# Optimization experiments

Hardware: AMD Instinct MI355X
Metric: run time of the kernel (lower is better)

The kernel has to match this reference:

```python
import jax, jax.numpy as jnp
import numpy as np

B, S, D, H = 16, 1024, 768, 12
HD = D // H
SCALE = HD ** -0.5


def setup_inputs() -> dict:
    key = jax.random.key(0)
    k1, k2, k3, k4 = jax.random.split(key, 4)
    # Xavier-uniform-like init for the linear weights
    lim_qkv = (6.0 / (D + 3 * D)) ** 0.5
    lim_proj = (6.0 / (D + D)) ** 0.5
    return {
        "hidden_states": jax.random.normal(k1, (B, S, D), dtype=jnp.float32),
        "mask": jax.random.randint(k2, (B, S), 0, 2).astype(bool),
        "qkv_w": jax.random.uniform(k3, (3 * D, D), minval=-lim_qkv, maxval=lim_qkv, dtype=jnp.float32),
        "qkv_b": jnp.zeros((3 * D,), dtype=jnp.float32),
        "proj_w": jax.random.uniform(k4, (D, D), minval=-lim_proj, maxval=lim_proj, dtype=jnp.float32),
        "proj_b": jnp.zeros((D,), dtype=jnp.float32),
    }


def _masked_softmax(scores, attn_mask):
    # scores: [B,H,S,S]; attn_mask: [B,1,S,S] bool. Fully-masked rows -> all-zero
    # weights (torch gives NaN there but then zeroes the output rows; zeroing
    # the weights yields the identical final output without NaNs).
    neg_inf = jnp.finfo(scores.dtype).min
    m = jnp.max(jnp.where(attn_mask, scores, neg_inf), axis=-1, keepdims=True)
    e = jnp.where(attn_mask, jnp.exp(scores - m), 0.0)
    denom = jnp.sum(e, axis=-1, keepdims=True)
    return e / jnp.where(denom == 0, 1.0, denom)


def reference(hidden_states, mask, qkv_w, qkv_b, proj_w, proj_b):
    # fused QKV projection: [B,S,3D]
    qkv = hidden_states @ qkv_w.T + qkv_b
    qkv = qkv.reshape(B, S, 3, H, HD).transpose(2, 0, 3, 1, 4)  # [3,B,H,S,hd]
    q, k, v = qkv[0], qkv[1], qkv[2]
    tok_mask = mask[:, None, :, None]  # [B,1,S,1]
    q = jnp.where(tok_mask, q, 0.0)
    k = jnp.where(tok_mask, k, 0.0)
    v = jnp.where(tok_mask, v, 0.0)
    scores = jnp.einsum("bhqd,bhkd->bhqk", q, k) * SCALE
    attn_mask = (mask[:, :, None] & mask[:, None, :])[:, None]  # [B,1,S,S]
    attn = _masked_softmax(scores, attn_mask)
    context = jnp.einsum("bhqk,bhkd->bhqd", attn, v)
    context = context.transpose(0, 2, 1, 3).reshape(B, S, D)
    out = context @ proj_w.T + proj_b
    out = jnp.where(mask[:, :, None], out, 0.0)
    return out
```

## Files before the change

### kernel.cpp

```cpp
#include <hip/hip_runtime.h>
#include <cstdint>
#include <cstddef>

#define B 16
#define S 1024
#define D 768
#define H 12
#define HD 64
#define NTOK (B * S)
#define QKV_N (3 * D)
#define SCALE 0.125f
#define C2 2.88539008f
#define GK 768
#define NT_K 12

typedef _Float16 f16x8 __attribute__((ext_vector_type(8)));
typedef _Float16 f16x4 __attribute__((ext_vector_type(4)));
typedef __fp16 fp16x2 __attribute__((ext_vector_type(2)));
typedef float f32x4 __attribute__((ext_vector_type(4)));

typedef __attribute__((address_space(3))) void as3_void;
typedef const __attribute__((address_space(1))) void as1_void;

#if defined(__has_builtin)
#if __has_builtin(__builtin_amdgcn_exp2f)
#define EXP2(x) __builtin_amdgcn_exp2f(x)
#else
#define EXP2(x) exp2f(x)
#endif
#else
#define EXP2(x) exp2f(x)
#endif

#define BARRIER() asm volatile("s_barrier" ::: "memory")

__global__ __launch_bounds__(256) void normalize_mask_kernel(
    const unsigned char* __restrict__ raw, int* __restrict__ outm, int n) {
    __shared__ int s_isbyte;
    const int tid = threadIdx.x;
    if (tid == 0) s_isbyte = 0;
    __syncthreads();
    int found = 0;
    for (int i = tid; i < n; i += 256) {
        if ((i & 3) != 0 && raw[i] != 0) found = 1;
    }
    if (found) atomicOr(&s_isbyte, 1);
    __syncthreads();
    const int isbyte = s_isbyte;
    if (isbyte) {
        for (int i = tid; i < n; i += 256) outm[i] = raw[i] ? 1 : 0;
    } else {
        const int* r32 = (const int*)raw;
        for (int i = tid; i < n; i += 256) outm[i] = r32[i] ? 1 : 0;
    }
}

__global__ __launch_bounds__(256) void cvt_all_f16(
    const float* __restrict__ in0, _Float16* __restrict__ out0, int n0,
    const float* __restrict__ in1, _Float16* __restrict__ out1, int n1,
    const float* __restrict__ in2, _Float16* __restrict__ out2, int n2) {
    int i = blockIdx.x * 256 + threadIdx.x;
    const float* in;
    _Float16* out;
    if (i < n0) { in = in0; out = out0; }
    else if (i < n0 + n1) { i -= n0; in = in1; out = out1; }
    else { i -= n0 + n1; in = in2; out = out2; if (i >= n2) return; }
    const float4 v = ((const float4*)in)[i];
    f16x4 o;
    o[0] = (_Float16)v.x; o[1] = (_Float16)v.y;
    o[2] = (_Float16)v.z; o[3] = (_Float16)v.w;
    ((f16x4*)out)[i] = o;
}

template <int MODE>
__global__ __launch_bounds__(256, 2) void gemm16(
    const _Float16* __restrict__ A, const _Float16* __restrict__ Wm,
    const float* __restrict__ bias, const int* __restrict__ rowmask,
    int N, float* __restrict__ outf, _Float16* __restrict__ outh,
    _Float16* __restrict__ vtb) {
    __shared__ _Float16 smem[32768];

    const int tid = threadIdx.x;
    const int w = tid >> 6, l = tid & 63;
    const int wm = (w >> 1) * 64, wn = (w & 1) * 64;
    const int lg = l >> 4, lc = l & 15;

    const int bid = blockIdx.x;
    const int xcd = bid & 7;
    const int idx = bid >> 3;
    const int bn = (idx >> 4) * 128;
    const int bm = (xcd * 16 + (idx & 15)) * 128;

    f32x4 acc[4][4] = {};

#define STAGE(T, BUF)                                                           \
    {                                                                           \
        const int kt_ = (T) * 64;                                               \
        _Pragma("unroll")                                                       \
        for (int i_ = 0; i_ < 4; ++i_) {                                        \
            const int ci_ = (w << 2) + i_;                           \
            const int r_ = (ci_ << 3) + (l >> 3);                               \
            const int c16_ = (l & 7) ^ (r_ & 7);                                \
            __builtin_amdgcn_global_load_lds(                                   \
                (as1_void*)(A + (size_t)(bm + r_) * GK + kt_ + c16_ * 8),       \
                (as3_void*)(smem + (BUF) * 8192 + ci_ * 512), 16, 0, 0);        \
            __builtin_amdgcn_global_load_lds(                                   \
                (as1_void*)(Wm + (size_t)(bn + r_) * GK + kt_ + c16_ * 8),      \
                (as3_void*)(smem + 16384 + (BUF) * 8192 + ci_ * 512), 16, 0, 0);\
        }                                                                       \
    }

    STAGE(0, 0)

    for (int t = 0; t < NT_K; ++t) {
        const int cur = t & 1;
        if (t + 1 < NT_K) {
            STAGE(t + 1, cur ^ 1)
            asm volatile("s_waitcnt vmcnt(8)" ::: "memory");
        } else {
            asm volatile("s_waitcnt vmcnt(0)" ::: "memory");
        }
        BARRIER();

        const _Float16* sA = smem + cur * 8192;
        const _Float16* sB = smem + 16384 + cur * 8192;
        __builtin_amdgcn_s_setprio(1);
#pragma unroll
        for (int kk = 0; kk < 2; ++kk) {
            const int c16 = ((kk << 2) + lg) ^ (lc & 7);
            f16x8 af[4], bf[4];
#pragma unroll
            for (int ni = 0; ni < 4; ++ni)
                bf[ni] = *(const f16x8*)&sB[(wn + ni * 16 + lc) * 64 + c16 * 8];
#pragma unroll
            for (int mi = 0; mi < 4; ++mi)
                af[mi] = *(const f16x8*)&sA[(wm + mi * 16 + lc) * 64 + c16 * 8];
#pragma unroll
            for (int mi = 0; mi < 4; ++mi)
#pragma unroll
                for (int ni = 0; ni < 4; ++ni)
                    acc[mi][ni] = __builtin_amdgcn_mfma_f32_16x16x32_f16(
                        af[mi], bf[ni], acc[mi][ni], 0, 0, 0);
        }
        __builtin_amdgcn_s_setprio(0);
        BARRIER();
    }
#undef STAGE

    float bs[4];
#pragma unroll
    for (int ni = 0; ni < 4; ++ni) bs[ni] = bias[bn + wn + ni * 16 + lc];

    if (MODE == 1) {
        if (bn < 1536) {
#pragma unroll
            for (int mi = 0; mi < 4; ++mi) {
#pragma unroll
                for (int j = 0; j < 4; ++j) {
                    const int m = bm + wm + mi * 16 + lg * 4 + j;
#pragma unroll
                    for (int ni = 0; ni < 4; ++ni) {
                        const int col = bn + wn + ni * 16 + lc;
                        outh[(size_t)m * N + col] =
                            (_Float16)(acc[mi][ni][j] + bs[ni]);
                    }
                }
            }
        } else {
#pragma unroll
            for (int mi = 0; mi < 4; ++mi) {
#pragma unroll
                for (int ni = 0; ni < 4; ++ni) {
                    f16x4 v4;
#pragma unroll
                    for (int j = 0; j < 4; ++j)
                        v4[j] = (_Float16)(acc[mi][ni][j] + bs[ni]);
                    const int nl = wn + ni * 16 + lc;
                    const int ml = wm + mi * 16 + lg * 4;
                    *(f16x4*)&smem[nl * 136 + ml] = v4;
                }
            }
            __syncthreads();
            const int r = tid >> 1;
            const int c0 = (tid & 1) * 64;
            const int col0 = bn - 1536 + r;
            const int hh = col0 >> 6, hd = col0 & 63;
            const int bb = bm >> 10;
            const int s0 = (bm & 1023) + c0;
            _Float16* dst = vtb + ((size_t)(bb * H + hh) * HD + hd) * S + s0;
#pragma unroll
            for (int e = 0; e < 8; ++e)
                *(f16x8*)(dst + e * 8) = *(const f16x8*)&smem[r * 136 + c0 + e * 8];
        }
    } else {
#pragma unroll
        for (int mi = 0; mi < 4; ++mi) {
#pragma unroll
            for (int j = 0; j < 4; ++j) {
                const int m = bm + wm + mi * 16 + lg * 4 + j;
                const int mv = rowmask[m];
#pragma unroll
                for (int ni = 0; ni < 4; ++ni) {
                    const int col = bn + wn + ni * 16 + lc;
                    outf[(size_t)m * N + col] = mv ? acc[mi][ni][j] + bs[ni] : 0.f;
                }
            }
        }
    }
}

__global__ __launch_bounds__(256, 3) void attn_kernel(
    const _Float16* __restrict__ qkv, const _Float16* __restrict__ vtb,
    const int* __restrict__ mask, _Float16* __restrict__ ctx) {
    __shared__ _Float16 ksm[3][64 * 64];
    __shared__ _Float16 vsm[3][64 * 64];
    __shared__ float mbias[S];

    const int blk = blockIdx.x;
    const int xcd = blk & 7;
    const int idx = blk >> 3;
    const int bh_ = xcd * 24 + (idx >> 2);
    const int qt = idx & 3;
    const int h = bh_ % H;
    const int b = bh_ / H;
    const int tid = threadIdx.x;
    const int w = tid >> 6, lane = tid & 63;
    const int lg = lane >> 4, lc = lane & 15;

    const size_t bh = (size_t)(b * H + h);
    const _Float16* Kp = qkv + (size_t)(b * S) * QKV_N + D + h * HD;
    const _Float16* Vt = vtb + bh * HD * S;
    const int* mrow = mask + b * S;

    const int r0 = w * 8 + (lane >> 3);
    const int swz8 = ((lane & 7) ^ (r0 & 7)) * 8;
    const int koff0 = r0 * QKV_N + swz8;
    const int koff1 = (32 + r0) * QKV_N + swz8;
    const int voff0 = r0 * S + swz8;
    const int voff1 = (32 + r0) * S + swz8;

#define STAGE(T, BUF)                                                          \
    {                                                                          \
        const int kt_ = (T) * 64;                                              \
        __builtin_amdgcn_global_load_lds(                                      \
            (as1_void*)(Kp + (size_t)kt_ * QKV_N + koff0),                     \
            (as3_void*)(&ksm[BUF][w * 512]), 16, 0, 0);                        \
        __builtin_amdgcn_global_load_lds(                                      \
            (as1_void*)(Kp + (size_t)kt_ * QKV_N + koff1),                     \
            (as3_void*)(&ksm[BUF][2048 + w * 512]), 16, 0, 0);                 \
        __builtin_amdgcn_global_load_lds(                                      \
            (as1_void*)(Vt + (size_t)kt_ + voff0),                            \
            (as3_void*)(&vsm[BUF][w * 512]), 16, 0, 0);                        \
        __builtin_amdgcn_global_load_lds(                                      \
            (as1_void*)(Vt + (size_t)kt_ + voff1),                            \
            (as3_void*)(&vsm[BUF][2048 + w * 512]), 16, 0, 0);                 \
    }

    const int qbase = qt * 256 + w * 16 + lc;
    const _Float16 qs = (_Float16)(0.125f * 1.44269504f);
    f16x8 qf[4][2];
#pragma unroll
    for (int qg = 0; qg < 4; ++qg) {
        const _Float16* Qp =
            qkv + (size_t)(b * S + qbase + qg * 64) * QKV_N + h * HD;
        qf[qg][0] = *(const f16x8*)(Qp + lg * 8);
        qf[qg][1] = *(const f16x8*)(Qp + 32 + lg * 8);
        qf[qg][0] *= qs;
        qf[qg][1] *= qs;
    }

#pragma unroll
    for (int i = 0; i < 4; ++i)
        mbias[i * 256 + tid] = mrow[i * 256 + tid] ? -C2 : -1e9f;

    STAGE(0, 0)
    STAGE(1, 1)

    f32x4 acc[4][4] = {};
    float lsum[4] = {0.f, 0.f, 0.f, 0.f};
    fp16x2 ones;
    ones[0] = (__fp16)1.0f; ones[1] = (__fp16)1.0f;

    int cur = 0;
    for (int it = 0; it < S / 64; ++it) {
        if (it + 2 < S / 64) {
            int nb = cur + 2; if (nb >= 3) nb -= 3;
            STAGE(it + 2, nb)
        }
        if (it == 0)
            asm volatile("s_waitcnt vmcnt(8) lgkmcnt(0)" ::: "memory");
        else if (it + 2 < S / 64)
            asm volatile("s_waitcnt vmcnt(8)" ::: "memory");
        else if (it + 2 == S / 64)
            asm volatile("s_waitcnt vmcnt(4)" ::: "memory");
        else
            asm volatile("s_waitcnt vmcnt(0)" ::: "memory");
        BARRIER();

        __builtin_amdgcn_s_setprio(1);
#pragma unroll
        for (int u = 0; u < 2; ++u) {
            f16x8 pp8[4];
#pragma unroll
            for (int s = 0; s < 2; ++s) {
                const int t = 2 * u + s;
                const int krow = (t * 16 + lc) * 64;
                const f16x8 kfa =
                    *(const f16x8*)&ksm[cur][krow + (lg ^ (lc & 7)) * 8];
                const f16x8 kfb =
                    *(const f16x8*)&ksm[cur][krow + ((4 + lg) ^ (lc & 7)) * 8];
                const f32x4 mb = *(const f32x4*)&mbias[it * 64 + t * 16 + 4 * lg];
#pragma unroll
                for (int qg = 0; qg < 4; ++qg) {
                    f32x4 c = mb;
                    c = __builtin_amdgcn_mfma_f32_16x16x32_f16(kfa, qf[qg][0], c, 0, 0, 0);
                    c = __builtin_amdgcn_mfma_f32_16x16x32_f16(kfb, qf[qg][1], c, 0, 0, 0);
                    const auto u0 = __builtin_amdgcn_cvt_pkrtz(EXP2(c[0]), EXP2(c[1]));
                    const auto u1 = __builtin_amdgcn_cvt_pkrtz(EXP2(c[2]), EXP2(c[3]));
                    lsum[qg] = __builtin_amdgcn_fdot2(u0, ones, lsum[qg], false);
                    lsum[qg] = __builtin_amdgcn_fdot2(u1, ones, lsum[qg], false);
                    pp8[qg][s * 4 + 0] = (_Float16)u0[0];
                    pp8[qg][s * 4 + 1] = (_Float16)u0[1];
                    pp8[qg][s * 4 + 2] = (_Float16)u1[0];
                    pp8[qg][s * 4 + 3] = (_Float16)u1[1];
                }
            }

#pragma unroll
            for (int g = 0; g < 4; ++g) {
                const int vrow = (g * 16 + lc) * 64;
                const int cA = ((4 * u + (lg >> 1)) ^ (lc & 7)) * 8 + (lg & 1) * 4;
                const int cB = ((4 * u + 2 + (lg >> 1)) ^ (lc & 7)) * 8 + (lg & 1) * 4;
                const f16x4 vlo = *(const f16x4*)&vsm[cur][vrow + cA];
                const f16x4 vhi = *(const f16x4*)&vsm[cur][vrow + cB];
                f16x8 vf8;
                vf8[0] = vlo[0]; vf8[1] = vlo[1]; vf8[2] = vlo[2]; vf8[3] = vlo[3];
                vf8[4] = vhi[0]; vf8[5] = vhi[1]; vf8[6] = vhi[2]; vf8[7] = vhi[3];
#pragma unroll
                for (int qg = 0; qg < 4; ++qg)
                    acc[qg][g] = __builtin_amdgcn_mfma_f32_16x16x32_f16(
                        pp8[qg], vf8, acc[qg][g], 0, 0, 0);
            }
        }
        __builtin_amdgcn_s_setprio(0);
        BARRIER();
        if (++cur >= 3) cur = 0;
    }
#undef STAGE

#pragma unroll
    for (int qg = 0; qg < 4; ++qg) {
        float l = lsum[qg];
        l += __shfl_xor(l, 16);
        l += __shfl_xor(l, 32);
        const float inv = l > 0.f ? 1.f / l : 0.f;
#pragma unroll
        for (int j = 0; j < 4; ++j) {
            const int qin = 4 * lg + j;
            const float ij = __shfl(inv, qin);
            const int qr = qt * 256 + qg * 64 + w * 16 + qin;
            const float iq = mrow[qr] ? ij : 0.f;
            const size_t o = ((size_t)(b * S + qr)) * D + h * HD;
#pragma unroll
            for (int g = 0; g < 4; ++g)
                ctx[o + 16 * g + lc] = (_Float16)(acc[qg][g][j] * iq);
        }
    }
}

extern "C" void kernel_launch(void* const* d_in, const int* in_sizes, int n_in,
                              void* d_out, int out_size, void* d_ws, size_t ws_size,
                              hipStream_t stream) {
    const float* hidden = (const float*)d_in[0];
    const unsigned char* maskraw = (const unsigned char*)d_in[1];
    const float* qkv_w = (const float*)d_in[2];
    const float* qkv_b = (const float*)d_in[3];
    const float* proj_w = (const float*)d_in[4];
    const float* proj_b = (const float*)d_in[5];
    float* out = (float*)d_out;

    char* ws = (char*)d_ws;
    size_t off = 0;
    int* maskN = (int*)(ws + off);            off += (size_t)NTOK * 4;
    _Float16* hid16 = (_Float16*)(ws + off);  off += (size_t)NTOK * D * 2;
    _Float16* qkvw16 = (_Float16*)(ws + off); off += (size_t)QKV_N * D * 2;
    _Float16* projw16 = (_Float16*)(ws + off); off += (size_t)D * D * 2;
    _Float16* qkv16 = (_Float16*)(ws + off);  off += (size_t)NTOK * QKV_N * 2;
    _Float16* vt = (_Float16*)(ws + off);     off += (size_t)NTOK * D * 2;
    _Float16* ctx16 = (_Float16*)(ws + off);  off += (size_t)NTOK * D * 2;

    normalize_mask_kernel<<<1, 256, 0, stream>>>(maskraw, maskN, NTOK);

    const int n0 = NTOK * D / 4, n1 = QKV_N * D / 4, n2 = D * D / 4;
    cvt_all_f16<<<(n0 + n1 + n2 + 255) / 256, 256, 0, stream>>>(
        hidden, hid16, n0, qkv_w, qkvw16, n1, proj_w, projw16, n2);

    gemm16<1><<<dim3(2304), 256, 0, stream>>>(
        hid16, qkvw16, qkv_b, nullptr, QKV_N, nullptr, qkv16, vt);

    attn_kernel<<<dim3(B * H * (S / 256)), 256, 0, stream>>>(qkv16, vt, maskN, ctx16);

    gemm16<0><<<dim3(768), 256, 0, stream>>>(
        ctx16, projw16, proj_b, maskN, D, out, nullptr, nullptr);
}
```

Measured before the change: 191.1 us.

## Use 256x256 tiles with 512 threads for QKV GEMM and pack softmax probabilities

The QKV projection GEMM moves from 128x128 tiles with 256 threads to 256x256 tiles with 8 waves, each computing 128x64. This raises arithmetic intensity and cuts the number of global loads per FLOP. The V-transpose epilogue now runs in two passes through shared memory. Separately, the attention kernel packs the cvt_pkrtz results as 32-bit ints instead of inserting individual halves, which should avoid per-element register shuffles. The larger tile uses 128KB of LDS and more accumulator registers per block, and gives only 576 blocks, which risks lower occupancy and weaker tail balance.

```diff
diff --git a/kernel.cpp b/kernel.cpp
--- a/kernel.cpp
+++ b/kernel.cpp
@@ -18,6 +18,7 @@
 typedef _Float16 f16x4 __attribute__((ext_vector_type(4)));
 typedef __fp16 fp16x2 __attribute__((ext_vector_type(2)));
 typedef float f32x4 __attribute__((ext_vector_type(4)));
+typedef int i32x4 __attribute__((ext_vector_type(4)));
 
 typedef __attribute__((address_space(3))) void as3_void;
 typedef const __attribute__((address_space(1))) void as1_void;
@@ -33,6 +34,9 @@
 #endif
 
 #define BARRIER() asm volatile("s_barrier" ::: "memory")
+
+union PPack { f16x8 h; i32x4 i; };
+union CPack { fp16x2 h; int i; };
 
 __global__ __launch_bounds__(256) void normalize_mask_kernel(
     const unsigned char* __restrict__ raw, int* __restrict__ outm, int n) {
@@ -72,12 +76,140 @@
     ((f16x4*)out)[i] = o;
 }
 
-template <int MODE>
-__global__ __launch_bounds__(256, 2) void gemm16(
+__global__ __launch_bounds__(512, 2) void gemm256(
+    const _Float16* __restrict__ A, const _Float16* __restrict__ Wm,
+    const float* __restrict__ bias, _Float16* __restrict__ outh,
+    _Float16* __restrict__ vtb) {
+    __shared__ _Float16 smem[65536];
+
+    const int tid = threadIdx.x;
+    const int w = tid >> 6, l = tid & 63;
+    const int wr = w >> 2, wc = w & 3;
+    const int wm = wr * 128, wn = wc * 64;
+    const int lg = l >> 4, lc = l & 15;
+
+    const int bid = blockIdx.x;
+    const int xcd = bid & 7;
+    const int idx = bid >> 3;
+    const int bn = (idx >> 3) * 256;
+    const int bm = (xcd * 8 + (idx & 7)) * 256;
+
+    const int r0 = l >> 3;
+    const int sw8 = ((l & 7) ^ (l >> 3)) * 8;
+
+    f32x4 acc[8][4] = {};
+
+#define STG(T, BUF)                                                            \
+    {                                                                          \
+        const int kt_ = (T) * 64;                                              \
+        _Float16* sA_ = smem + (BUF) * 16384;                                  \
+        _Float16* sB_ = smem + 32768 + (BUF) * 16384;                          \
+        _Pragma("unroll")                                                      \
+        for (int i_ = 0; i_ < 4; ++i_) {                                       \
+            const int seg_ = i_ * 8 + w;                                       \
+            const int rr_ = seg_ * 8 + r0;                                     \
+            __builtin_amdgcn_global_load_lds(                                  \
+                (as1_void*)(A + (size_t)(bm + rr_) * GK + kt_ + sw8),          \
+                (as3_void*)(sA_ + seg_ * 512), 16, 0, 0);                      \
+            __builtin_amdgcn_global_load_lds(                                  \
+                (as1_void*)(Wm + (size_t)(bn + rr_) * GK + kt_ + sw8),         \
+                (as3_void*)(sB_ + seg_ * 512), 16, 0, 0);                      \
+        }                                                                      \
+    }
+
+    STG(0, 0)
+
+    for (int t = 0; t < NT_K; ++t) {
+        const int cur = t & 1;
+        if (t + 1 < NT_K) {
+            STG(t + 1, cur ^ 1)
+            asm volatile("s_waitcnt vmcnt(8)" ::: "memory");
+        } else {
+            asm volatile("s_waitcnt vmcnt(0)" ::: "memory");
+        }
+        BARRIER();
+
+        const _Float16* sA = smem + cur * 16384;
+        const _Float16* sB = smem + 32768 + cur * 16384;
+        __builtin_amdgcn_s_setprio(1);
+#pragma unroll
+        for (int kk = 0; kk < 2; ++kk) {
+            const int c16 = ((kk << 2) + lg) ^ (lc & 7);
+            f16x8 bf[4], af[8];
+#pragma unroll
+            for (int ni = 0; ni < 4; ++ni)
+                bf[ni] = *(const f16x8*)&sB[(wn + ni * 16 + lc) * 64 + c16 * 8];
+#pragma unroll
+            for (int mi = 0; mi < 8; ++mi)
+                af[mi] = *(const f16x8*)&sA[(wm + mi * 16 + lc) * 64 + c16 * 8];
+#pragma unroll
+            for (int mi = 0; mi < 8; ++mi)
+#pragma unroll
+                for (int ni = 0; ni < 4; ++ni)
+                    acc[mi][ni] = __builtin_amdgcn_mfma_f32_16x16x32_f16(
+                        af[mi], bf[ni], acc[mi][ni], 0, 0, 0);
+        }
+        __builtin_amdgcn_s_setprio(0);
+        BARRIER();
+    }
+#undef STG
+
+    float bs[4];
+#pragma unroll
+    for (int ni = 0; ni < 4; ++ni) bs[ni] = bias[bn + wn + ni * 16 + lc];
+
+    if (bn < 1536) {
+#pragma unroll
+        for (int mi = 0; mi < 8; ++mi) {
+#pragma unroll
+            for (int j = 0; j < 4; ++j) {
+                const int m = bm + wm + mi * 16 + lg * 4 + j;
+#pragma unroll
+                for (int ni = 0; ni < 4; ++ni) {
+                    const int col = bn + wn + ni * 16 + lc;
+                    outh[(size_t)m * QKV_N + col] =
+                        (_Float16)(acc[mi][ni][j] + bs[ni]);
+                }
+            }
+        }
+    } else {
+#pragma unroll
+        for (int p = 0; p < 2; ++p) {
+            BARRIER();
+            if ((wc >> 1) == p) {
+#pragma unroll
+                for (int mi = 0; mi < 8; ++mi) {
+#pragma unroll
+                    for (int ni = 0; ni < 4; ++ni) {
+                        f16x4 v4;
+#pragma unroll
+                        for (int j = 0; j < 4; ++j)
+                            v4[j] = (_Float16)(acc[mi][ni][j] + bs[ni]);
+                        const int cl = wn - p * 128 + ni * 16 + lc;
+                        const int row = wm + mi * 16 + lg * 4;
+                        *(f16x4*)&smem[cl * 264 + row] = v4;
+                    }
+                }
+            }
+            BARRIER();
+            const int r = tid >> 2;
+            const int c0 = (tid & 3) * 64;
+            const int col0 = bn - 1536 + p * 128 + r;
+            const int hh = col0 >> 6, hd = col0 & 63;
+            const int bb = bm >> 10;
+            const int s0 = (bm & 1023) + c0;
+            _Float16* dst = vtb + ((size_t)(bb * H + hh) * HD + hd) * S + s0;
+#pragma unroll
+            for (int e = 0; e < 8; ++e)
+                *(f16x8*)(dst + e * 8) = *(const f16x8*)&smem[r * 264 + c0 + e * 8];
+        }
+    }
+}
+
+__global__ __launch_bounds__(256, 2) void gemm_proj(
     const _Float16* __restrict__ A, const _Float16* __restrict__ Wm,
     const float* __restrict__ bias, const int* __restrict__ rowmask,
-    int N, float* __restrict__ outf, _Float16* __restrict__ outh,
-    _Float16* __restrict__ vtb) {
+    float* __restrict__ outf) {
     __shared__ _Float16 smem[32768];
 
     const int tid = threadIdx.x;
@@ -98,7 +230,7 @@
         const int kt_ = (T) * 64;                                               \
         _Pragma("unroll")                                                       \
         for (int i_ = 0; i_ < 4; ++i_) {                                        \
-            const int ci_ = (w << 2) + i_;                           \
+            const int ci_ = (w << 2) + i_;                                      \
             const int r_ = (ci_ << 3) + (l >> 3);                               \
             const int c16_ = (l & 7) ^ (r_ & 7);                                \
             __builtin_amdgcn_global_load_lds(                                   \
@@ -151,59 +283,16 @@
 #pragma unroll
     for (int ni = 0; ni < 4; ++ni) bs[ni] = bias[bn + wn + ni * 16 + lc];
 
-    if (MODE == 1) {
-        if (bn < 1536) {
-#pragma unroll
-            for (int mi = 0; mi < 4; ++mi) {
-#pragma unroll
-                for (int j = 0; j < 4; ++j) {
-                    const int m = bm + wm + mi * 16 + lg * 4 + j;
-#pragma unroll
-                    for (int ni = 0; ni < 4; ++ni) {
-                        const int col = bn + wn + ni * 16 + lc;
-                        outh[(size_t)m * N + col] =
-                            (_Float16)(acc[mi][ni][j] + bs[ni]);
-                    }
-                }
-            }
-        } else {
-#pragma unroll
-            for (int mi = 0; mi < 4; ++mi) {
-#pragma unroll
-                for (int ni = 0; ni < 4; ++ni) {
-                    f16x4 v4;
-#pragma unroll
-                    for (int j = 0; j < 4; ++j)
-                        v4[j] = (_Float16)(acc[mi][ni][j] + bs[ni]);
-                    const int nl = wn + ni * 16 + lc;
-                    const int ml = wm + mi * 16 + lg * 4;
-                    *(f16x4*)&smem[nl * 136 + ml] = v4;
-                }
-            }
-            __syncthreads();
-            const int r = tid >> 1;
-            const int c0 = (tid & 1) * 64;
-            const int col0 = bn - 1536 + r;
-            const int hh = col0 >> 6, hd = col0 & 63;
-            const int bb = bm >> 10;
-            const int s0 = (bm & 1023) + c0;
-            _Float16* dst = vtb + ((size_t)(bb * H + hh) * HD + hd) * S + s0;
-#pragma unroll
-            for (int e = 0; e < 8; ++e)
-                *(f16x8*)(dst + e * 8) = *(const f16x8*)&smem[r * 136 + c0 + e * 8];
-        }
-    } else {
-#pragma unroll
-        for (int mi = 0; mi < 4; ++mi) {
-#pragma unroll
-            for (int j = 0; j < 4; ++j) {
-                const int m = bm + wm + mi * 16 + lg * 4 + j;
-                const int mv = rowmask[m];
-#pragma unroll
-                for (int ni = 0; ni < 4; ++ni) {
-                    const int col = bn + wn + ni * 16 + lc;
-                    outf[(size_t)m * N + col] = mv ? acc[mi][ni][j] + bs[ni] : 0.f;
-                }
+#pragma unroll
+    for (int mi = 0; mi < 4; ++mi) {
+#pragma unroll
+        for (int j = 0; j < 4; ++j) {
+            const int m = bm + wm + mi * 16 + lg * 4 + j;
+            const int mv = rowmask[m];
+#pragma unroll
+            for (int ni = 0; ni < 4; ++ni) {
+                const int col = bn + wn + ni * 16 + lc;
+                outf[(size_t)m * D + col] = mv ? acc[mi][ni][j] + bs[ni] : 0.f;
             }
         }
     }
@@ -300,7 +389,7 @@
         __builtin_amdgcn_s_setprio(1);
 #pragma unroll
         for (int u = 0; u < 2; ++u) {
-            f16x8 pp8[4];
+            PPack pp8[4];
 #pragma unroll
             for (int s = 0; s < 2; ++s) {
                 const int t = 2 * u + s;
@@ -315,14 +404,13 @@
                     f32x4 c = mb;
                     c = __builtin_amdgcn_mfma_f32_16x16x32_f16(kfa, qf[qg][0], c, 0, 0, 0);
                     c = __builtin_amdgcn_mfma_f32_16x16x32_f16(kfb, qf[qg][1], c, 0, 0, 0);
-                    const auto u0 = __builtin_amdgcn_cvt_pkrtz(EXP2(c[0]), EXP2(c[1]));
-                    const auto u1 = __builtin_amdgcn_cvt_pkrtz(EXP2(c[2]), EXP2(c[3]));
-                    lsum[qg] = __builtin_amdgcn_fdot2(u0, ones, lsum[qg], false);
-                    lsum[qg] = __builtin_amdgcn_fdot2(u1, ones, lsum[qg], false);
-                    pp8[qg][s * 4 + 0] = (_Float16)u0[0];
-                    pp8[qg][s * 4 + 1] = (_Float16)u0[1];
-                    pp8[qg][s * 4 + 2] = (_Float16)u1[0];
-                    pp8[qg][s * 4 + 3] = (_Float16)u1[1];
+                    CPack u0, u1;
+                    u0.h = __builtin_amdgcn_cvt_pkrtz(EXP2(c[0]), EXP2(c[1]));
+                    u1.h = __builtin_amdgcn_cvt_pkrtz(EXP2(c[2]), EXP2(c[3]));
+                    lsum[qg] = __builtin_amdgcn_fdot2(u0.h, ones, lsum[qg], false);
+                    lsum[qg] = __builtin_amdgcn_fdot2(u1.h, ones, lsum[qg], false);
+                    pp8[qg].i[s * 2 + 0] = u0.i;
+                    pp8[qg].i[s * 2 + 1] = u1.i;
                 }
             }
 
@@ -339,7 +427,7 @@
 #pragma unroll
                 for (int qg = 0; qg < 4; ++qg)
                     acc[qg][g] = __builtin_amdgcn_mfma_f32_16x16x32_f16(
-                        pp8[qg], vf8, acc[qg][g], 0, 0, 0);
+                        pp8[qg].h, vf8, acc[qg][g], 0, 0, 0);
             }
         }
         __builtin_amdgcn_s_setprio(0);
@@ -395,11 +483,9 @@
     cvt_all_f16<<<(n0 + n1 + n2 + 255) / 256, 256, 0, stream>>>(
         hidden, hid16, n0, qkv_w, qkvw16, n1, proj_w, projw16, n2);
 
-    gemm16<1><<<dim3(2304), 256, 0, stream>>>(
-        hid16, qkvw16, qkv_b, nullptr, QKV_N, nullptr, qkv16, vt);
+    gemm256<<<dim3(576), 512, 0, stream>>>(hid16, qkvw16, qkv_b, qkv16, vt);
 
     attn_kernel<<<dim3(B * H * (S / 256)), 256, 0, stream>>>(qkv16, vt, maskN, ctx16);
 
-    gemm16<0><<<dim3(768), 256, 0, stream>>>(
-        ctx16, projw16, proj_b, maskN, D, out, nullptr, nullptr);
-}
+    gemm_proj<<<dim3(768), 256, 0, stream>>>(ctx16, projw16, proj_b, maskN, out);
+}
```

Result: slower. 215.8 us (+12.9%).
